# Kernel optimization log

Measured on AMD Instinct MI355X. Metric: run time of the kernel, lower is better.

Reference implementation:

```python
import jax, jax.numpy as jnp
import numpy as np

P, Q = 8, 8  # patch_size


def _patchify(x):
    # x: [b, c, H, W] -> patches [b, h*w, c*p*q]
    b, c, H, W = x.shape
    h, w = H // P, W // Q
    x = x.reshape(b, c, h, P, w, Q)
    x = x.transpose(0, 2, 4, 1, 3, 5)  # b h w c p q
    return x.reshape(b, h * w, c * P * Q)


def _depatchify(patches, c, H, W):
    # patches: [b, h*w, c*p*q] -> [b, c, H, W]
    b = patches.shape[0]
    h, w = H // P, W // Q
    x = patches.reshape(b, h, w, c, P, Q)
    x = x.transpose(0, 3, 1, 4, 2, 5)  # b c h p w q
    return x.reshape(b, c, H, W)


def setup_inputs() -> dict:
    key = jax.random.key(0)
    x = jax.random.normal(key, (16, 3, 512, 512), dtype=jnp.float32)
    return {"x": x, "rank": 32}


def reference(x, rank):
    b, c, H, W = x.shape
    patches = _patchify(x)  # [b, N, D] with N = (H/8)*(W/8), D = c*64
    u, s, vt = jnp.linalg.svd(patches, full_matrices=False)
    u = u[..., :rank]          # [b, N, r]
    s = s[..., :rank]          # [b, r]
    vt = vt[..., :rank, :]     # [b, r, D]
    # original: u*sqrt(s), v = sqrt(s)*vt^T; reconstruction u @ v^T == (u*s) @ vt
    recon = (u * s[..., None, :]) @ vt  # [b, N, D]
    return _depatchify(recon, c, H, W)
```

## Files before the change

### kernel.cpp

```cpp
#include <hip/hip_runtime.h>
#include <cstdint>
#include <cstddef>

#define IMG 512
#define JD 192

__device__ inline float fast_rcp(float x) { return __builtin_amdgcn_rcpf(x); }

__global__ __launch_bounds__(512) void k_gram(const float* __restrict__ x,
                                              float* __restrict__ part) {
  const int ck = blockIdx.x;
  const int sl = blockIdx.y;
  const int b  = blockIdx.z;
  const int t  = threadIdx.x;
  __shared__ float tile[32][JD];
  __shared__ float pacc[256*37];
  const int g   = t >> 8;
  const int tid = t & 255;
  const int ty = tid >> 5;
  const int tx = tid & 31;
  const int r0 = sl*48 + ty*6;
  const int c0 = tx*6;
  float acc[6][6];
#pragma unroll
  for (int i=0;i<6;i++)
#pragma unroll
    for (int j=0;j<6;j++) acc[i][j]=0.f;
  const float* xb = x + (size_t)b*3*IMG*IMG;
  const int nbeg = ck*1024;
  const int nlo = g*16, nhi = nlo+16;
  for (int n0 = nbeg; n0 < nbeg+1024; n0 += 32) {
    for (int f = t; f < 32*JD; f += 512) {
      const int nl = f / JD, j = f - nl*JD;
      const int n = n0 + nl;
      const int hh = n >> 6, ww = n & 63;
      const int c = j >> 6, p = (j >> 3) & 7, q = j & 7;
      tile[nl][j] = xb[(c*IMG + hh*8+p)*IMG + ww*8 + q];
    }
    __syncthreads();
#pragma unroll 4
    for (int nl = nlo; nl < nhi; nl++) {
      const float2 a01 = *(const float2*)(&tile[nl][r0]);
      const float2 a23 = *(const float2*)(&tile[nl][r0+2]);
      const float2 a45 = *(const float2*)(&tile[nl][r0+4]);
      const float2 b01 = *(const float2*)(&tile[nl][c0]);
      const float2 b23 = *(const float2*)(&tile[nl][c0+2]);
      const float2 b45 = *(const float2*)(&tile[nl][c0+4]);
      const float va[6] = {a01.x,a01.y,a23.x,a23.y,a45.x,a45.y};
      const float vb[6] = {b01.x,b01.y,b23.x,b23.y,b45.x,b45.y};
#pragma unroll
      for (int i=0;i<6;i++)
#pragma unroll
        for (int j=0;j<6;j++) acc[i][j] += va[i]*vb[j];
    }
    __syncthreads();
  }
  if (g == 1) {
#pragma unroll
    for (int i=0;i<6;i++)
#pragma unroll
      for (int j=0;j<6;j++) pacc[tid*37 + i*6+j] = acc[i][j];
  }
  __syncthreads();
  if (g == 0) {
    float* dst = part + (((size_t)(b*4 + sl))*4 + ck) * (size_t)(48*JD);
#pragma unroll
    for (int i=0;i<6;i++)
#pragma unroll
      for (int j=0;j<6;j++)
        dst[(ty*6+i)*JD + c0+j] = acc[i][j] + pacc[tid*37 + i*6+j];
  }
}

__global__ __launch_bounds__(256) void k_greduce(const float* __restrict__ part,
                                                 float* __restrict__ Gs) {
  const int idx = blockIdx.x*256 + threadIdx.x;
  const int b = idx / (JD*JD);
  const int e = idx - b*(JD*JD);
  const int r = e / JD;
  const int sl = r / 48;
  const int w = (r - sl*48)*JD + (e - r*JD);
  const float* p = part + ((size_t)(b*4+sl))*4*(48*JD) + w;
  float s = 0.f;
#pragma unroll
  for (int ck=0; ck<4; ck++) s += p[(size_t)ck*48*JD];
  Gs[idx] = s * (1.0f/4096.0f);
}

__global__ __launch_bounds__(256) void k_sq(const float* __restrict__ S,
                                            float* __restrict__ D) {
  const int tp = blockIdx.x;
  const int b  = blockIdx.y;
  int ti, tj;
  if      (tp==0){ti=0;tj=0;} else if (tp==1){ti=1;tj=0;}
  else if (tp==2){ti=1;tj=1;} else if (tp==3){ti=2;tj=0;}
  else if (tp==4){ti=2;tj=1;} else            {ti=2;tj=2;}
  const float* Sb = S + (size_t)b*JD*JD;
  float* Db = D + (size_t)b*JD*JD;
  __shared__ float Ar[64][33];
  __shared__ float Br[64][33];
  const int t = threadIdx.x;
  const int ty = t >> 4, tx = t & 15;
  float acc[4][4];
#pragma unroll
  for (int i=0;i<4;i++)
#pragma unroll
    for (int j=0;j<4;j++) acc[i][j]=0.f;
  for (int k0=0; k0<JD; k0+=32) {
    for (int f=t; f<2048; f+=256) {
      const int row = f >> 5, kk = f & 31;
      Ar[row][kk] = Sb[(ti*64+row)*JD + k0+kk];
      Br[row][kk] = Sb[(tj*64+row)*JD + k0+kk];
    }
    __syncthreads();
#pragma unroll 4
    for (int k=0;k<32;k++) {
      float va[4], vb[4];
#pragma unroll
      for (int i=0;i<4;i++) va[i] = Ar[ty*4+i][k];
#pragma unroll
      for (int j=0;j<4;j++) vb[j] = Br[tx*4+j][k];
#pragma unroll
      for (int i=0;i<4;i++)
#pragma unroll
        for (int j=0;j<4;j++) acc[i][j] += va[i]*vb[j];
    }
    __syncthreads();
  }
#pragma unroll
  for (int i=0;i<4;i++)
#pragma unroll
    for (int j=0;j<4;j++) {
      const int r = ti*64+ty*4+i, c = tj*64+tx*4+j;
      Db[r*JD+c] = acc[i][j];
      if (ti != tj) Db[c*JD+r] = acc[i][j];
    }
}


__device__ void orth_lds(float* __restrict__ Wl, float* __restrict__ S1,
                         float* __restrict__ rdv, float* __restrict__ pdv,
                         float* __restrict__ misc, int t, float ridge) {
  const int ty = t >> 5, tx = t & 31;
  float acc[4][2];
#pragma unroll
  for (int i=0;i<4;i++)
#pragma unroll
    for (int j=0;j<2;j++) acc[i][j]=0.f;
  __syncthreads();
#pragma unroll 2
  for (int r=0; r<JD; r++) {
    const float4 va4 = *(const float4*)(Wl + r*68 + ty*4);
    const float2 vb2 = *(const float2*)(Wl + r*68 + tx*2);
    const float a4[4] = {va4.x, va4.y, va4.z, va4.w};
    const float b2[2] = {vb2.x, vb2.y};
#pragma unroll
    for (int i=0;i<4;i++)
#pragma unroll
      for (int j=0;j<2;j++) acc[i][j] += a4[i]*b2[j];
  }
#pragma unroll
  for (int i=0;i<4;i++)
#pragma unroll
    for (int j=0;j<2;j++)
      S1[(ty*4+i)*68 + tx*2+j] = acc[i][j];
  __syncthreads();
  if (ridge > 0.f) {
    if (t < 64) {
      float d = S1[t*68+t];
#pragma unroll
      for (int o=1;o<64;o<<=1) d = fmaxf(d, __shfl_xor(d, o));
      if (t == 0) misc[0] = d * ridge;
    }
    __syncthreads();
    if (t < 64) S1[t*68+t] += misc[0];
    __syncthreads();
  }
  for (int p=0; p<4; p++) {
    const int b16 = p*16;
    if (t < 64) {
      for (int jj=0; jj<16; jj++) {
        const int j = b16 + jj;
        const float invd = fast_rcp(S1[j*68+j]);
        if (t == 0) pdv[jj] = invd;
        const int nit = (15-jj)*16;
        for (int f=t; f<nit; f+=64) {
          const int i = j+1 + (f>>4);
          const int k = j+1 + (f&15);
          if (k <= i)
            S1[i*68+k] -= S1[i*68+j]*S1[k*68+j]*invd;
        }
      }
    }
    __syncthreads();
    const int rb = b16 + 16;
    if (t < 64 - rb) {
      const int r = rb + t;
      float pr[16];
      float4* prp = (float4*)pr;
      prp[0] = *(const float4*)(S1 + r*68 + b16);
      prp[1] = *(const float4*)(S1 + r*68 + b16 + 4);
      prp[2] = *(const float4*)(S1 + r*68 + b16 + 8);
      prp[3] = *(const float4*)(S1 + r*68 + b16 + 12);
#pragma unroll
      for (int c=1; c<16; c++) {
        float s = pr[c];
#pragma unroll
        for (int j=0; j<c; j++) s -= pr[j]*S1[(b16+c)*68 + b16+j]*pdv[j];
        pr[c] = s;
      }
      *(float4*)(S1 + r*68 + b16)      = prp[0];
      *(float4*)(S1 + r*68 + b16 + 4)  = prp[1];
      *(float4*)(S1 + r*68 + b16 + 8)  = prp[2];
      *(float4*)(S1 + r*68 + b16 + 12) = prp[3];
    }
    __syncthreads();
    for (int f=t; f<2304; f+=512) {
      const int i = rb + f/48;
      const int k = rb + (f - (f/48)*48);
      if (i < 64 && k < 64 && k <= i) {
        float s = S1[i*68+k];
#pragma unroll
        for (int jj=0; jj<16; jj++)
          s -= S1[i*68 + b16+jj]*S1[k*68 + b16+jj]*pdv[jj];
        S1[i*68+k] = s;
      }
    }
    __syncthreads();
  }
  if (t < 64) rdv[t] = rsqrtf(S1[t*68+t]);
  __syncthreads();
  for (int f=t; f<4096; f+=512) {
    const int i = f>>6, k = f&63;
    if (k < i) S1[i*68+k] *= rdv[k];
  }
  __syncthreads();
  if (t < JD) {
    float w[64];
    float4* wp = (float4*)w;
#pragma unroll
    for (int c4=0;c4<16;c4++) wp[c4] = *(const float4*)(Wl + t*68 + c4*4);
#pragma unroll
    for (int c=0;c<64;c++) {
      float v = w[c];
#pragma unroll
      for (int k=0;k<c;k++) v -= w[k]*S1[c*68+k];
      w[c] = v * rdv[c];
    }
#pragma unroll
    for (int c4=0;c4<16;c4++) *(float4*)(Wl + t*68 + c4*4) = wp[c4];
  }
  __syncthreads();
}

__device__ void mm_lds(const float* __restrict__ G, const float* __restrict__ Win,
                       float* __restrict__ Wout, float* __restrict__ Gt, int t) {
  const int rg = t >> 3;
  const int cg = t & 7;
  float acc[3][8];
#pragma unroll
  for (int i=0;i<3;i++)
#pragma unroll
    for (int j=0;j<8;j++) acc[i][j]=0.f;
  for (int k0=0; k0<JD; k0+=32) {
    __syncthreads();
    for (int f=t; f<6144; f+=512) {
      const int r = f >> 5, kk = f & 31;
      Gt[kk*193 + r] = G[r*JD + k0 + kk];
    }
    __syncthreads();
#pragma unroll 2
    for (int k=0;k<32;k++) {
      const float a0 = Gt[k*193 + rg*3+0];
      const float a1 = Gt[k*193 + rg*3+1];
      const float a2 = Gt[k*193 + rg*3+2];
      const float* wr = Win + (k0+k)*68 + cg*8;
#pragma unroll
      for (int j4=0;j4<2;j4++) {
        const float4 b4 = *(const float4*)(wr + 4*j4);
        const float bb[4] = {b4.x, b4.y, b4.z, b4.w};
#pragma unroll
        for (int jj=0;jj<4;jj++) {
          acc[0][j4*4+jj] += a0*bb[jj];
          acc[1][j4*4+jj] += a1*bb[jj];
          acc[2][j4*4+jj] += a2*bb[jj];
        }
      }
    }
  }
  __syncthreads();
#pragma unroll
  for (int i=0;i<3;i++)
#pragma unroll
    for (int j=0;j<8;j++)
      Wout[(rg*3+i)*68 + cg*8 + j] = acc[i][j];
  __syncthreads();
}

__device__ void hgemm_lds(const float* __restrict__ X, const float* __restrict__ Y,
                          float* __restrict__ S1, int ss, int t) {
  const int ty = t >> 5, tx = t & 31;
  float acc[4][2];
#pragma unroll
  for (int i=0;i<4;i++)
#pragma unroll
    for (int j=0;j<2;j++) acc[i][j]=0.f;
#pragma unroll 2
  for (int r=0; r<JD; r++) {
    const float4 va4 = *(const float4*)(X + r*68 + ty*4);
    const float2 vb2 = *(const float2*)(Y + r*68 + tx*2);
    const float a4[4] = {va4.x, va4.y, va4.z, va4.w};
    const float b2[2] = {vb2.x, vb2.y};
#pragma unroll
    for (int i=0;i<4;i++)
#pragma unroll
      for (int j=0;j<2;j++) acc[i][j] += a4[i]*b2[j];
  }
  __syncthreads();
#pragma unroll
  for (int i=0;i<4;i++)
#pragma unroll
    for (int j=0;j<2;j++)
      S1[(ty*4+i)*ss + tx*2+j] = acc[i][j];
  __syncthreads();
}

__global__ __launch_bounds__(512) void k_subH(const float* __restrict__ G32g,
                                              const float* __restrict__ Gsg,
                                              float* __restrict__ WbG,
                                              float* __restrict__ Hgg) {
  const int b = blockIdx.x;
  const int t = threadIdx.x;
  __shared__ float W0l[192*68];
  __shared__ float W1l[192*68];
  __shared__ float scr[32*193];
  __shared__ float rdv[64];
  __shared__ float pdv[16];
  __shared__ float misc[8];
  const float* Gb  = G32g + (size_t)b*JD*JD;
  const float* Gsb = Gsg  + (size_t)b*JD*JD;

  for (int f=t; f<JD*64; f+=512)
    W0l[(f>>6)*68 + (f&63)] = Gb[(f>>6)*JD + (f&63)];
  __syncthreads();

  orth_lds(W0l, scr, rdv, pdv, misc, t, 1e-6f);
  mm_lds(Gb, W0l, W1l, scr, t);
  orth_lds(W1l, scr, rdv, pdv, misc, t, 1e-6f);
  orth_lds(W1l, scr, rdv, pdv, misc, t, 0.f);

  mm_lds(Gsb, W1l, W0l, scr, t);
  hgemm_lds(W1l, W0l, scr, 65, t);

  float* Wb = WbG + (size_t)b*JD*64;
  for (int f=t; f<JD*64; f+=512)
    Wb[f] = W1l[(f>>6)*68 + (f&63)];
  float* Hb = Hgg + (size_t)b*4160;
  for (int f=t; f<4160; f+=512) Hb[f] = scr[f];
}

__device__ void dev_tridiag(float* __restrict__ A, float* a, float* b2,
                            float* bsg, float* v0s, float* bts,
                            float* vvec, float* wvec, int t) {
  for (int j=0; j<=61; j++) {
    const int m = 63 - j;
    if (t < 64) {
      float xi = (t < m) ? A[j*65 + (j+1+t)] : 0.f;
      float nr = xi*xi;
#pragma unroll
      for (int o=1;o<64;o<<=1) nr += __shfl_xor(nr, o);
      const float sig = sqrtf(nr);
      const float alpha = __shfl(xi, 0);
      const float sgn = (alpha >= 0.f) ? 1.f : -1.f;
      const float v0 = alpha + sgn*sig;
      const float beta = (sig > 1e-20f) ? 1.0f/(sig*fabsf(v0)) : 0.f;
      if (t < m) vvec[t] = (t==0) ? v0 : xi;
      if (t == 0) {
        a[j] = A[j*65+j]; b2[j] = nr; bsg[j] = -sgn*sig;
        v0s[j] = v0; bts[j] = beta;
      }
      float pv = 0.f;
      if (t < m) {
        const float* row = A + (j+1+t)*65 + (j+1);
        for (int c=0;c<m;c++) pv += row[c]*vvec[c];
        pv *= beta;
      }
      float dp = (t<m) ? vvec[t]*pv : 0.f;
#pragma unroll
      for (int o=1;o<64;o<<=1) dp += __shfl_xor(dp, o);
      const float gamma = 0.5f*beta*dp;
      if (t < m) wvec[t] = pv - gamma*vvec[t];
    }
    __syncthreads();
    const int mm = m*m;
    for (int f=t; f<mm; f+=256) {
      const int r = f/m, c = f - r*m;
      A[(j+1+r)*65 + (j+1+c)] -= vvec[r]*wvec[c] + wvec[r]*vvec[c];
    }
    __syncthreads();
  }
  if (t == 0) {
    a[62] = A[62*65+62];
    a[63] = A[63*65+63];
    const float bb = A[62*65+63];
    b2[62] = bb*bb;
    bsg[62] = bb;
  }
  __syncthreads();
}

__device__ inline int sturm_cnt_fast(const float* a, const float* b2, float sig) {
  float d = a[0] - sig;
  int n = (d < 0.f) ? 1 : 0;
#pragma unroll 8
  for (int i=1;i<64;i++) {
    const float dd = (fabsf(d) < 1e-20f) ? -1e-20f : d;
    d = (a[i]-sig) - b2[i-1]*fast_rcp(dd);
    n += (d < 0.f) ? 1 : 0;
  }
  return n;
}

__device__ inline float dguard(float d) {
  if (fabsf(d) < 1e-12f) return (d < 0.f) ? -1e-12f : 1e-12f;
  return d;
}

__global__ __launch_bounds__(256) void k_eigv(const float* __restrict__ Hgg,
                                              float* __restrict__ VtG) {
  const int b = blockIdx.x;
  const int t = threadIdx.x;
  __shared__ float SH[4160];
  __shared__ float Vt[64*36];
  __shared__ float dpA[64*33];
  __shared__ float dmA[64*33];
  __shared__ float ps[8*33];
  __shared__ float wvred[32];
  __shared__ float rdv[64];
  __shared__ float a64[64];
  __shared__ float b2v[64];
  __shared__ float bsg[64];
  __shared__ float v0s[64];
  __shared__ float bts[64];
  __shared__ float vvec[64];
  __shared__ float wvec[64];
  __shared__ float lam[32];
  __shared__ float misc[8];
  const float* Hb = Hgg + (size_t)b*4160;
  for (int f=t; f<4160; f+=256) SH[f] = Hb[f];
  __syncthreads();

  dev_tridiag(SH, a64, b2v, bsg, v0s, bts, vvec, wvec, t);

  if (t < 64) {
    const float bl = (t>0)  ? sqrtf(b2v[t-1]) : 0.f;
    const float br = (t<63) ? sqrtf(b2v[t])   : 0.f;
    float lo = a64[t] - bl - br, hi = a64[t] + bl + br;
#pragma unroll
    for (int o=1;o<64;o<<=1) {
      lo = fminf(lo, __shfl_xor(lo,o));
      hi = fmaxf(hi, __shfl_xor(hi,o));
    }
    if (t == 0) { misc[0] = lo - 1e-4f; misc[1] = hi + 1e-4f; }
  }
  __syncthreads();

  {
    const int l = t >> 3, g = t & 7;
    const int r = 32 + l;
    float L = misc[0], H = misc[1];
    for (int it=0; it<10; it++) {
      const float mid = L + (H-L)*((float)(g+1)*(1.0f/9.0f));
      const int cnt = sturm_cnt_fast(a64, b2v, mid);
      float nL = L, nH = H;
#pragma unroll
      for (int k=0;k<8;k++) {
        const int ck = __shfl(cnt, k, 8);
        const float pk = L + (H-L)*((float)(k+1)*(1.0f/9.0f));
        if (ck <= r) nL = fmaxf(nL, pk); else nH = fminf(nH, pk);
      }
      L = nL; H = nH;
    }
    if (g == 0) lam[l] = 0.5f*(L+H);
  }
  __syncthreads();

  if (t < 32) {
    const int l = t;
    const float lm = lam[l];
    float d = dguard(a64[0] - lm);
    dpA[0*33+l] = d;
    for (int i=1;i<64;i++) {
      d = dguard((a64[i]-lm) - b2v[i-1]*fast_rcp(d));
      dpA[i*33+l] = d;
    }
    float e = dguard(a64[63] - lm);
    dmA[63*33+l] = e;
    for (int i=62;i>=0;i--) {
      e = dguard((a64[i]-lm) - b2v[i]*fast_rcp(e));
      dmA[i*33+l] = e;
    }
    int ks = 0; float gbest = 1e30f;
    for (int i=0;i<64;i++) {
      const float g = fabsf(dpA[i*33+l] + dmA[i*33+l] - (a64[i]-lm));
      if (g < gbest) { gbest = g; ks = i; }
    }
    Vt[ks*36+l] = 1.f;
    float z = 1.f;
    for (int i=ks-1;i>=0;i--) {
      z = -(bsg[i]*z) * fast_rcp(dpA[i*33+l]);
      z = fminf(fmaxf(z, -1e18f), 1e18f);
      Vt[i*36+l] = z;
    }
    z = 1.f;
    for (int i=ks+1;i<64;i++) {
      z = -(bsg[i-1]*z) * fast_rcp(dmA[i*33+l]);
      z = fminf(fmaxf(z, -1e18f), 1e18f);
      Vt[i*36+l] = z;
    }
    float nr2 = 0.f;
    for (int i=0;i<64;i++) { const float zz = Vt[i*36+l]; nr2 += zz*zz; }
    const float inv = rsqrtf(nr2);
    for (int i=0;i<64;i++) Vt[i*36+l] *= inv;
  }
  __syncthreads();

  for (int f=t; f<1024; f+=256) {
    const int i = f>>5, j = f&31;
    float s = 0.f;
    for (int r=0;r<64;r++) s += Vt[r*36+i]*Vt[r*36+j];
    dpA[i*33+j] = s;
  }
  __syncthreads();
  if (t == 0) {
    float m = 0.f;
    for (int j=0;j<32;j++) m = fmaxf(m, dpA[j*33+j]);
    misc[2] = m * 1e-7f;
  }
  __syncthreads();
  if (t < 32) dpA[t*33+t] += misc[2];
  for (int j=0;j<31;j++) {
    __syncthreads();
    const float invd = fast_rcp(dpA[j*33+j]);
    for (int f=t; f<(31-j)*32; f+=256) {
      const int i = j+1 + (f>>5);
      const int k = f & 31;
      if (k > j && k <= i)
        dpA[i*33+k] -= dpA[i*33+j]*dpA[k*33+j]*invd;
    }
  }
  __syncthreads();
  if (t < 32) rdv[t] = rsqrtf(dpA[t*33+t]);
  __syncthreads();
  for (int f=t; f<1024; f+=256) {
    const int i = f>>5, k = f&31;
    if (k < i) dpA[i*33+k] *= rdv[k];
  }
  __syncthreads();
  if (t < 64) {
    float w[32];
#pragma unroll
    for (int c=0;c<32;c++) w[c] = Vt[t*36+c];
#pragma unroll
    for (int c=0;c<32;c++) {
      float v = w[c];
#pragma unroll
      for (int k=0;k<c;k++) v -= w[k]*dpA[c*33+k];
      w[c] = v * rdv[c];
    }
#pragma unroll
    for (int c=0;c<32;c++) Vt[t*36+c] = w[c];
  }
  __syncthreads();

  for (int j=61; j>=0; j--) {
    const int m = 63 - j;
    {
      const int c = t & 31, g = t >> 5;
      float s = 0.f;
      for (int r=g; r<m; r+=8) {
        const float vr = (r==0) ? v0s[j] : SH[j*65 + (j+1+r)];
        s += vr * Vt[(j+1+r)*36 + c];
      }
      ps[g*33+c] = s;
    }
    __syncthreads();
    if (t < 32) {
      float s = 0.f;
#pragma unroll
      for (int g=0;g<8;g++) s += ps[g*33+t];
      wvred[t] = s * bts[j];
    }
    __syncthreads();
    {
      const int c = t & 31, g = t >> 5;
      for (int r=g; r<m; r+=8) {
        const float vr = (r==0) ? v0s[j] : SH[j*65 + (j+1+r)];
        Vt[(j+1+r)*36 + c] -= vr * wvred[c];
      }
    }
    __syncthreads();
  }

  float* Vb = VtG + (size_t)b*2048;
  for (int f=t; f<2048; f+=256) Vb[f] = Vt[(f>>5)*36 + (f&31)];
}

__global__ __launch_bounds__(256) void k_bv(const float* __restrict__ WbG,
                                            const float* __restrict__ VtG,
                                            float* __restrict__ Btg) {
  const int b = blockIdx.x;
  const int t = threadIdx.x;
  __shared__ float Vt[64*36];
  const float* W = WbG + (size_t)b*JD*64;
  const float* Vb = VtG + (size_t)b*2048;
  float* Bt = Btg + (size_t)b*32*JD;
  for (int f=t; f<2048; f+=256) Vt[(f>>5)*36 + (f&31)] = Vb[f];
  __syncthreads();
  if (t < JD) {
    float accv[32];
#pragma unroll
    for (int c=0;c<32;c++) accv[c] = 0.f;
    const float4* crow = (const float4*)(W + t*64);
#pragma unroll 2
    for (int kb=0; kb<16; kb++) {
      const float4 av = crow[kb];
      const float a4[4] = {av.x, av.y, av.z, av.w};
#pragma unroll
      for (int ki=0; ki<4; ki++) {
        const float aa = a4[ki];
        const float* vrow = Vt + (kb*4+ki)*36;
        const float4 v0 = *(const float4*)(vrow+0);
        const float4 v1 = *(const float4*)(vrow+4);
        const float4 v2 = *(const float4*)(vrow+8);
        const float4 v3 = *(const float4*)(vrow+12);
        const float4 v4 = *(const float4*)(vrow+16);
        const float4 v5 = *(const float4*)(vrow+20);
        const float4 v6 = *(const float4*)(vrow+24);
        const float4 v7 = *(const float4*)(vrow+28);
        accv[0]+=aa*v0.x; accv[1]+=aa*v0.y; accv[2]+=aa*v0.z; accv[3]+=aa*v0.w;
        accv[4]+=aa*v1.x; accv[5]+=aa*v1.y; accv[6]+=aa*v1.z; accv[7]+=aa*v1.w;
        accv[8]+=aa*v2.x; accv[9]+=aa*v2.y; accv[10]+=aa*v2.z; accv[11]+=aa*v2.w;
        accv[12]+=aa*v3.x; accv[13]+=aa*v3.y; accv[14]+=aa*v3.z; accv[15]+=aa*v3.w;
        accv[16]+=aa*v4.x; accv[17]+=aa*v4.y; accv[18]+=aa*v4.z; accv[19]+=aa*v4.w;
        accv[20]+=aa*v5.x; accv[21]+=aa*v5.y; accv[22]+=aa*v5.z; accv[23]+=aa*v5.w;
        accv[24]+=aa*v6.x; accv[25]+=aa*v6.y; accv[26]+=aa*v6.z; accv[27]+=aa*v6.w;
        accv[28]+=aa*v7.x; accv[29]+=aa*v7.y; accv[30]+=aa*v7.z; accv[31]+=aa*v7.w;
      }
    }
#pragma unroll
    for (int c=0;c<32;c++) Bt[c*JD + t] = accv[c];
  }
}

__global__ __launch_bounds__(256) void k_mm(const float* __restrict__ Btg,
                                            float* __restrict__ Mg) {
  const int tp = blockIdx.x;
  const int b  = blockIdx.y;
  int ti, tj;
  if      (tp==0){ti=0;tj=0;} else if (tp==1){ti=1;tj=0;}
  else if (tp==2){ti=1;tj=1;} else if (tp==3){ti=2;tj=0;}
  else if (tp==4){ti=2;tj=1;} else            {ti=2;tj=2;}
  const float* Bt = Btg + (size_t)b*32*JD;
  float* Mb = Mg + (size_t)b*JD*JD;
  __shared__ float Ar[32][68];
  __shared__ float Br[32][68];
  const int t = threadIdx.x;
  const int ty = t >> 4, tx = t & 15;
  for (int f=t; f<2048; f+=256) {
    const int k = f >> 6, c = f & 63;
    Ar[k][c] = Bt[k*JD + ti*64 + c];
    Br[k][c] = Bt[k*JD + tj*64 + c];
  }
  __syncthreads();
  float acc[4][4];
#pragma unroll
  for (int i=0;i<4;i++)
#pragma unroll
    for (int j=0;j<4;j++) acc[i][j]=0.f;
#pragma unroll 4
  for (int k=0;k<32;k++) {
    const float4 va4 = *(const float4*)(&Ar[k][ty*4]);
    const float4 vb4 = *(const float4*)(&Br[k][tx*4]);
    const float a4[4] = {va4.x, va4.y, va4.z, va4.w};
    const float b4[4] = {vb4.x, vb4.y, vb4.z, vb4.w};
#pragma unroll
    for (int i=0;i<4;i++)
#pragma unroll
      for (int j=0;j<4;j++) acc[i][j] += a4[i]*b4[j];
  }
#pragma unroll
  for (int i=0;i<4;i++)
#pragma unroll
    for (int j=0;j<4;j++) {
      const int r = ti*64+ty*4+i, c = tj*64+tx*4+j;
      Mb[r*JD+c] = acc[i][j];
      if (ti != tj) Mb[c*JD+r] = acc[i][j];
    }
}

__global__ __launch_bounds__(256) void k_recon(const float* __restrict__ x,
                                               const float* __restrict__ Mg,
                                               float* __restrict__ out) {
  const int nb = blockIdx.x;
  const int b  = blockIdx.y;
  const int t  = threadIdx.x;
  __shared__ float At[32][17];
  __shared__ float Mt[16][JD];
  const float* xb = x + (size_t)b*3*IMG*IMG;
  const float* Mb = Mg + (size_t)b*JD*JD;
  float* ob = out + (size_t)b*3*IMG*IMG;
  const int pg = t >> 4;
  const int jg = t & 15;
  float acc[2][12];
#pragma unroll
  for (int i=0;i<2;i++)
#pragma unroll
    for (int j=0;j<12;j++) acc[i][j]=0.f;
  for (int j0=0; j0<JD; j0+=16) {
    for (int f=t; f<512; f+=256) {
      const int nl = f >> 4, jj = f & 15;
      const int j = j0 + jj;
      const int n = nb*32 + nl;
      const int hh = n >> 6, ww = n & 63;
      const int c = j >> 6, p = (j >> 3) & 7, q = j & 7;
      At[nl][jj] = xb[(c*IMG + hh*8+p)*IMG + ww*8 + q];
    }
    for (int f=t; f<768; f+=256) {
      const int jj = f/48, cc = (f - jj*48)*4;
      *(float4*)(&Mt[jj][cc]) = *(const float4*)(Mb + (size_t)(j0+jj)*JD + cc);
    }
    __syncthreads();
#pragma unroll 4
    for (int jj=0;jj<16;jj++) {
      const float a0 = At[pg*2+0][jj];
      const float a1 = At[pg*2+1][jj];
      const float4 m0 = *(const float4*)(&Mt[jj][jg*12]);
      const float4 m1 = *(const float4*)(&Mt[jj][jg*12+4]);
      const float4 m2 = *(const float4*)(&Mt[jj][jg*12+8]);
      const float mm[12] = {m0.x,m0.y,m0.z,m0.w,m1.x,m1.y,m1.z,m1.w,
                            m2.x,m2.y,m2.z,m2.w};
#pragma unroll
      for (int j=0;j<12;j++) {
        acc[0][j] += a0*mm[j];
        acc[1][j] += a1*mm[j];
      }
    }
    __syncthreads();
  }
#pragma unroll
  for (int i=0;i<2;i++) {
    const int n = nb*32 + pg*2 + i;
    const int hh = n >> 6, ww = n & 63;
#pragma unroll
    for (int j4=0;j4<3;j4++) {
      const int jo = jg*12 + j4*4;
      const int c = jo >> 6, p = (jo >> 3) & 7, q = jo & 7;
      const float4 v = make_float4(acc[i][j4*4+0], acc[i][j4*4+1],
                                   acc[i][j4*4+2], acc[i][j4*4+3]);
      *(float4*)(ob + (size_t)(c*IMG + hh*8+p)*IMG + ww*8 + q) = v;
    }
  }
}

extern "C" void kernel_launch(void* const* d_in, const int* in_sizes, int n_in,
                              void* d_out, int out_size, void* d_ws, size_t ws_size,
                              hipStream_t stream) {
  (void)in_sizes; (void)n_in; (void)out_size; (void)ws_size;
  const float* x = (const float*)d_in[0];
  float* out = (float*)d_out;
  float* ws  = (float*)d_ws;

  float* part = ws;
  float* Gs   = ws + 2359296;
  float* P0   = ws + 2949120;
  float* P1   = ws + 3538944;
  float* Mg   = ws;
  float* Wb   = ws + 786432;
  float* Hg   = ws + 983040;
  float* Vtg  = ws + 1057792;
  float* Btg  = ws + 1090560;

  k_gram  <<<dim3(4,4,16), 512, 0, stream>>>(x, part);
  k_greduce<<<2304,        256, 0, stream>>>(part, Gs);
  k_sq    <<<dim3(6,16),   256, 0, stream>>>(Gs, P0);
  k_sq    <<<dim3(6,16),   256, 0, stream>>>(P0, P1);
  k_sq    <<<dim3(6,16),   256, 0, stream>>>(P1, P0);
  k_sq    <<<dim3(6,16),   256, 0, stream>>>(P0, P1);
  k_sq    <<<dim3(6,16),   256, 0, stream>>>(P1, P0);
  k_subH  <<<16,           512, 0, stream>>>(P0, Gs, Wb, Hg);
  k_eigv  <<<16,           256, 0, stream>>>(Hg, Vtg);
  k_bv    <<<16,           256, 0, stream>>>(Wb, Vtg, Btg);
  k_mm    <<<dim3(6,16),   256, 0, stream>>>(Btg, Mg);
  k_recon <<<dim3(128,16), 256, 0, stream>>>(x, Mg, out);
}
```

Measured before the change: 953.8 us.

## Double-buffer Gram tile loads with float4 register prefetch

The Gram kernel now keeps two shared-memory tiles and prefetches the next 32-row chunk into registers with float4 global loads while computing on the current tile. The next tile is written to shared memory after the compute, which removes one barrier per iteration. The gather is also vectorised from scalar loads with index divisions to precomputed float4 offsets. This costs more LDS and registers, which may lower occupancy.

```diff
diff --git a/kernel.cpp b/kernel.cpp
--- a/kernel.cpp
+++ b/kernel.cpp
@@ -13,7 +13,7 @@
   const int sl = blockIdx.y;
   const int b  = blockIdx.z;
   const int t  = threadIdx.x;
-  __shared__ float tile[32][JD];
+  __shared__ float tile[2][32][JD];
   __shared__ float pacc[256*37];
   const int g   = t >> 8;
   const int tid = t & 255;
@@ -29,23 +29,47 @@
   const float* xb = x + (size_t)b*3*IMG*IMG;
   const int nbeg = ck*1024;
   const int nlo = g*16, nhi = nlo+16;
-  for (int n0 = nbeg; n0 < nbeg+1024; n0 += 32) {
-    for (int f = t; f < 32*JD; f += 512) {
-      const int nl = f / JD, j = f - nl*JD;
-      const int n = n0 + nl;
-      const int hh = n >> 6, ww = n & 63;
-      const int c = j >> 6, p = (j >> 3) & 7, q = j & 7;
-      tile[nl][j] = xb[(c*IMG + hh*8+p)*IMG + ww*8 + q];
-    }
-    __syncthreads();
+
+  int snl[3]; size_t cpo[3]; float* wp0[3];
+#pragma unroll
+  for (int k=0;k<3;k++) {
+    const int f = t + k*512;
+    const int nl = f/48, j4 = f - nl*48;
+    const int c = j4 >> 4, p = (j4 >> 1) & 7, q = (j4 & 1)*4;
+    snl[k] = nl;
+    cpo[k] = (size_t)(c*IMG + p)*IMG + q;
+    wp0[k] = &tile[0][nl][j4*4];
+  }
+  float4 regs[3];
+#pragma unroll
+  for (int k=0;k<3;k++) {
+    const int n = nbeg + snl[k];
+    regs[k] = *(const float4*)(xb + cpo[k] + (size_t)(n>>6)*8*IMG + (n&63)*8);
+  }
+#pragma unroll
+  for (int k=0;k<3;k++) *(float4*)wp0[k] = regs[k];
+  __syncthreads();
+
+  int cur = 0;
+  for (int it=0; it<32; it++) {
+    if (it < 31) {
+      const int n0 = nbeg + (it+1)*32;
+#pragma unroll
+      for (int k=0;k<3;k++) {
+        const int n = n0 + snl[k];
+        regs[k] = *(const float4*)(xb + cpo[k] + (size_t)(n>>6)*8*IMG + (n&63)*8);
+      }
+    }
+    const float* tb = &tile[cur][0][0];
 #pragma unroll 4
     for (int nl = nlo; nl < nhi; nl++) {
-      const float2 a01 = *(const float2*)(&tile[nl][r0]);
-      const float2 a23 = *(const float2*)(&tile[nl][r0+2]);
-      const float2 a45 = *(const float2*)(&tile[nl][r0+4]);
-      const float2 b01 = *(const float2*)(&tile[nl][c0]);
-      const float2 b23 = *(const float2*)(&tile[nl][c0+2]);
-      const float2 b45 = *(const float2*)(&tile[nl][c0+4]);
+      const float* tr = tb + nl*JD;
+      const float2 a01 = *(const float2*)(tr + r0);
+      const float2 a23 = *(const float2*)(tr + r0+2);
+      const float2 a45 = *(const float2*)(tr + r0+4);
+      const float2 b01 = *(const float2*)(tr + c0);
+      const float2 b23 = *(const float2*)(tr + c0+2);
+      const float2 b45 = *(const float2*)(tr + c0+4);
       const float va[6] = {a01.x,a01.y,a23.x,a23.y,a45.x,a45.y};
       const float vb[6] = {b01.x,b01.y,b23.x,b23.y,b45.x,b45.y};
 #pragma unroll
@@ -53,7 +77,12 @@
 #pragma unroll
         for (int j=0;j<6;j++) acc[i][j] += va[i]*vb[j];
     }
-    __syncthreads();
+    if (it < 31) {
+#pragma unroll
+      for (int k=0;k<3;k++) *(float4*)(wp0[k] + (cur^1)*6144) = regs[k];
+    }
+    __syncthreads();
+    cur ^= 1;
   }
   if (g == 1) {
 #pragma unroll
```

Measured after the change: 862.2 us. 9.6% less time.
